# Performance work log

Hardware: AMD Instinct MI355X
Metric: run time of the kernel (lower is better)

## Reference

```python
import jax, jax.numpy as jnp
import numpy as np

B, S, D, H = 4, 2048, 2048, 16
HD = D // H          # 128, head_dim
THETA = 10000.0


def _rope_cos_sin(seq_len, head_dim, theta, dtype):
    # angle[t, j] = t * theta ** (-2j / head_dim), j = 0..head_dim//2-1
    inv_freq = theta ** (-jnp.arange(0, head_dim, 2, dtype=jnp.float32) / head_dim)
    ang = jnp.arange(seq_len, dtype=jnp.float32)[:, None] * inv_freq[None, :]  # [S, HD/2]
    # broadcast over heads: [S, 1, HD/2]
    return jnp.cos(ang)[:, None, :].astype(dtype), jnp.sin(ang)[:, None, :].astype(dtype)


def _apply_rope(t, cos, sin):
    # t: [B, S, H, HD]; complex mult on adjacent pairs (even=real, odd=imag)
    tr, ti = t[..., 0::2], t[..., 1::2]              # [B, S, H, HD/2]
    or_ = tr * cos - ti * sin
    oi_ = tr * sin + ti * cos
    return jnp.stack([or_, oi_], axis=-1).reshape(t.shape)


def setup_inputs() -> dict:
    key = jax.random.key(0)
    k1, k2, k3, k4, k5 = jax.random.split(key, 5)
    s = 1.0 / np.sqrt(D)
    return {
        "x": jax.random.normal(k1, (B, S, D), jnp.float32),
        "Wqkv": jax.random.normal(k2, (3 * D, D), jnp.float32) * s,
        "bqkv": jax.random.normal(k3, (3 * D,), jnp.float32) * 0.01,
        "Wo": jax.random.normal(k4, (D, D), jnp.float32) * s,
        "bo": jax.random.normal(k5, (D,), jnp.float32) * 0.01,
    }


def reference(x, Wqkv, bqkv, Wo, bo):
    b, s, d = x.shape
    qkv = x @ Wqkv.T + bqkv                          # [B, S, 3D]
    q, k, v = jnp.split(qkv, 3, axis=-1)
    q = q.reshape(b, s, H, HD)
    k = k.reshape(b, s, H, HD)
    v = v.reshape(b, s, H, HD)

    cos, sin = _rope_cos_sin(s, HD, THETA, x.dtype)
    q = _apply_rope(q, cos, sin)
    k = _apply_rope(k, cos, sin)

    # causal SDPA, scale = 1/sqrt(head_dim)
    scale = 1.0 / jnp.sqrt(jnp.asarray(HD, x.dtype))
    scores = jnp.einsum('bqhd,bkhd->bhqk', q, k) * scale
    causal = jnp.tril(jnp.ones((s, s), bool))
    scores = jnp.where(causal[None, None], scores, jnp.asarray(-jnp.inf, x.dtype))
    attn = jax.nn.softmax(scores, axis=-1)
    o = jnp.einsum('bhqk,bkhd->bqhd', attn, v).reshape(b, s, d)
    return o @ Wo.T + bo
```

## Files before the change

kernel.cpp:

```cpp
#include <hip/hip_runtime.h>
#include <hip/hip_bf16.h>
#include <math.h>

#define B_   4
#define S_   2048
#define D_   2048
#define H_   16
#define HD_  128
#define N3_  6144
#define M_   8192

typedef __attribute__((ext_vector_type(8))) short  short8;
typedef __attribute__((ext_vector_type(4))) float  float4_;

using bf16 = __hip_bfloat16;

static __device__ __forceinline__ float bf2f(bf16 v){ return __bfloat162float(v); }
static __device__ __forceinline__ bf16  f2bf(float v){ return __float2bfloat16(v); }
static __device__ __forceinline__ short f2bfs(float v){
    return (short)__builtin_bit_cast(unsigned short, __float2bfloat16(v));
}

static __device__ __forceinline__ short8 load8(const bf16* p){ return *(const short8*)p; }
static __device__ __forceinline__ short8 load8(const float* p){
    float4_ a = *(const float4_*)p;
    float4_ b = *(const float4_*)(p + 4);
    short8 r;
    r[0]=f2bfs(a[0]); r[1]=f2bfs(a[1]); r[2]=f2bfs(a[2]); r[3]=f2bfs(a[3]);
    r[4]=f2bfs(b[0]); r[5]=f2bfs(b[1]); r[6]=f2bfs(b[2]); r[7]=f2bfs(b[3]);
    return r;
}

static __device__ __forceinline__ void cp16_g2l(const void* g, void* l){
    __builtin_amdgcn_global_load_lds((const __attribute__((address_space(1))) void*)g,
                                     (__attribute__((address_space(3))) void*)l,
                                     16, 0, 0);
}

#define MFMA16 __builtin_amdgcn_mfma_f32_16x16x32_bf16

__global__ void cast_f32_bf16(const float* __restrict__ in, bf16* __restrict__ out, long n8){
    long i = (long)blockIdx.x * blockDim.x + threadIdx.x;
    if (i >= n8) return;
    *((short8*)out + i) = load8(in + 8*i);
}

template<typename AT, typename BT, typename OUT_T>
__global__ __launch_bounds__(256) void gemm_bt(const AT* __restrict__ A, int lda,
                                               const BT* __restrict__ Bt, int ldb,
                                               const float* __restrict__ bias,
                                               OUT_T* __restrict__ C, int ldc, int Kdim){
    __shared__ __align__(16) bf16 As[128*32];
    __shared__ __align__(16) bf16 Bs[128*32];
    const int tid  = threadIdx.x;
    const int lane = tid & 63;
    const int w    = tid >> 6;
    const int wm   = w >> 1, wn = w & 1;
    const int quad = lane >> 4, l15 = lane & 15;
    const int bn0  = blockIdx.x * 128, bm0 = blockIdx.y * 128;
    const int srow = tid >> 2;
    const int scol = (tid & 3) * 8;

    float4_ acc[4][4] = {};

    for (int k0 = 0; k0 < Kdim; k0 += 32){
        __syncthreads();
        #pragma unroll
        for (int half = 0; half < 2; ++half){
            int r = half*64 + srow;
            *(short8*)&As[r*32 + scol] = load8(&A[(size_t)(bm0 + r)*lda + k0 + scol]);
            *(short8*)&Bs[r*32 + scol] = load8(&Bt[(size_t)(bn0 + r)*ldb + k0 + scol]);
        }
        __syncthreads();
        short8 af[4], bfr[4];
        #pragma unroll
        for (int mt = 0; mt < 4; ++mt) af[mt]  = *(const short8*)&As[(wm*64 + mt*16 + l15)*32 + quad*8];
        #pragma unroll
        for (int nt = 0; nt < 4; ++nt) bfr[nt] = *(const short8*)&Bs[(wn*64 + nt*16 + l15)*32 + quad*8];
        #pragma unroll
        for (int mt = 0; mt < 4; ++mt)
            #pragma unroll
            for (int nt = 0; nt < 4; ++nt)
                acc[mt][nt] = MFMA16(af[mt], bfr[nt], acc[mt][nt], 0, 0, 0);
    }

    #pragma unroll
    for (int mt = 0; mt < 4; ++mt){
        int row = bm0 + wm*64 + mt*16 + quad*4;
        #pragma unroll
        for (int nt = 0; nt < 4; ++nt){
            int col = bn0 + wn*64 + nt*16 + l15;
            float bia = bias[col];
            #pragma unroll
            for (int r = 0; r < 4; ++r){
                float v = acc[mt][nt][r] + bia;
                size_t idx = (size_t)(row + r)*ldc + col;
                if constexpr (sizeof(OUT_T) == 2) ((bf16*)C)[idx] = f2bf(v);
                else                              ((float*)C)[idx] = v;
            }
        }
    }
}

template<typename OUT_T>
__global__ __launch_bounds__(512, 2) void gemm256(const bf16* __restrict__ A, int lda,
                                                  const bf16* __restrict__ Bt, int ldb,
                                                  const float* __restrict__ bias,
                                                  OUT_T* __restrict__ C, int ldc, int Kdim){
    __shared__ __align__(16) char lds[131072];
    const int tid  = threadIdx.x;
    const int lane = tid & 63;
    const int w    = tid >> 6;
    const int wm   = w >> 2, wn = w & 3;
    const int quad = lane >> 4, l15 = lane & 15;
    const int sw   = l15 & 7;
    const int bn0  = blockIdx.x * 256, bm0 = blockIdx.y * 256;

    const int g1 = tid, g2 = tid + 512;
    const int r1 = g1 >> 3, c1 = g1 & 7;
    const int r2 = g2 >> 3, c2 = g2 & 7;
    const int d1 = g1 * 16, d2 = g2 * 16;
    const char* pA0g1 = (const char*)(A  + (size_t)(bm0 +       r1)*lda + ((c1 ^ (r1 & 7)) << 3));
    const char* pA0g2 = (const char*)(A  + (size_t)(bm0 +       r2)*lda + ((c2 ^ (r2 & 7)) << 3));
    const char* pA1g1 = (const char*)(A  + (size_t)(bm0 + 128 + r1)*lda + ((c1 ^ (r1 & 7)) << 3));
    const char* pA1g2 = (const char*)(A  + (size_t)(bm0 + 128 + r2)*lda + ((c2 ^ (r2 & 7)) << 3));
    const char* pB0g1 = (const char*)(Bt + (size_t)(bn0 +       r1)*ldb + ((c1 ^ (r1 & 7)) << 3));
    const char* pB0g2 = (const char*)(Bt + (size_t)(bn0 +       r2)*ldb + ((c2 ^ (r2 & 7)) << 3));
    const char* pB1g1 = (const char*)(Bt + (size_t)(bn0 + 128 + r1)*ldb + ((c1 ^ (r1 & 7)) << 3));
    const char* pB1g2 = (const char*)(Bt + (size_t)(bn0 + 128 + r2)*ldb + ((c2 ^ (r2 & 7)) << 3));

    auto STAGE = [&](int bufb, int kby){
        cp16_g2l(pA0g1 + kby, lds + bufb +         d1);
        cp16_g2l(pA0g2 + kby, lds + bufb +         d2);
        cp16_g2l(pA1g1 + kby, lds + bufb + 16384 + d1);
        cp16_g2l(pA1g2 + kby, lds + bufb + 16384 + d2);
        cp16_g2l(pB0g1 + kby, lds + bufb + 32768 + d1);
        cp16_g2l(pB0g2 + kby, lds + bufb + 32768 + d2);
        cp16_g2l(pB1g1 + kby, lds + bufb + 49152 + d1);
        cp16_g2l(pB1g2 + kby, lds + bufb + 49152 + d2);
    };

    const int abase = (wm ? 16384 : 0);
    const int bbase = 32768 + ((wn >> 1) ? 16384 : 0);
    const int brow0 = (wn & 1) * 64;
    auto LDA = [&](int bufb, int mt, int kk) -> short8 {
        return *(const short8*)(lds + bufb + abase + (mt*16 + l15)*128
                                + (((kk*4 + quad) ^ sw) << 4));
    };
    auto LDB = [&](int bufb, int nt, int kk) -> short8 {
        return *(const short8*)(lds + bufb + bbase + (brow0 + nt*16 + l15)*128
                                + (((kk*4 + quad) ^ sw) << 4));
    };

    float4_ acc[8][4] = {};
    const int NT = Kdim >> 6;

    STAGE(0, 0);
    asm volatile("s_waitcnt vmcnt(0)" ::: "memory");
    __builtin_amdgcn_s_barrier();

    int cur = 0;
    for (int kt = 0; kt < NT; ++kt){
        const int bufb = cur << 16;
        if (kt + 1 < NT){
            STAGE(bufb ^ 65536, (kt + 1) << 7);
            asm volatile("s_waitcnt vmcnt(8)" ::: "memory");
        } else {
            asm volatile("s_waitcnt vmcnt(0)" ::: "memory");
        }
        __builtin_amdgcn_s_barrier();

        short8 af[4][2], bf[2][2], bg[2][2];
        #pragma unroll
        for (int mt = 0; mt < 4; ++mt){ af[mt][0] = LDA(bufb, mt, 0); af[mt][1] = LDA(bufb, mt, 1); }
        #pragma unroll
        for (int nt = 0; nt < 2; ++nt){ bf[nt][0] = LDB(bufb, nt, 0); bf[nt][1] = LDB(bufb, nt, 1); }
        __builtin_amdgcn_s_setprio(1);
        #pragma unroll
        for (int mt = 0; mt < 4; ++mt)
            #pragma unroll
            for (int nt = 0; nt < 2; ++nt){
                acc[mt][nt] = MFMA16(af[mt][0], bf[nt][0], acc[mt][nt], 0, 0, 0);
                acc[mt][nt] = MFMA16(af[mt][1], bf[nt][1], acc[mt][nt], 0, 0, 0);
            }
        __builtin_amdgcn_s_setprio(0);
        __builtin_amdgcn_s_barrier();
        #pragma unroll
        for (int nt = 0; nt < 2; ++nt){ bg[nt][0] = LDB(bufb, nt + 2, 0); bg[nt][1] = LDB(bufb, nt + 2, 1); }
        __builtin_amdgcn_s_setprio(1);
        #pragma unroll
        for (int mt = 0; mt < 4; ++mt)
            #pragma unroll
            for (int nt = 0; nt < 2; ++nt){
                acc[mt][nt+2] = MFMA16(af[mt][0], bg[nt][0], acc[mt][nt+2], 0, 0, 0);
                acc[mt][nt+2] = MFMA16(af[mt][1], bg[nt][1], acc[mt][nt+2], 0, 0, 0);
            }
        __builtin_amdgcn_s_setprio(0);
        __builtin_amdgcn_s_barrier();
        #pragma unroll
        for (int mt = 0; mt < 4; ++mt){ af[mt][0] = LDA(bufb, mt + 4, 0); af[mt][1] = LDA(bufb, mt + 4, 1); }
        __builtin_amdgcn_s_setprio(1);
        #pragma unroll
        for (int mt = 0; mt < 4; ++mt)
            #pragma unroll
            for (int nt = 0; nt < 2; ++nt){
                acc[mt+4][nt+2] = MFMA16(af[mt][0], bg[nt][0], acc[mt+4][nt+2], 0, 0, 0);
                acc[mt+4][nt+2] = MFMA16(af[mt][1], bg[nt][1], acc[mt+4][nt+2], 0, 0, 0);
            }
        __builtin_amdgcn_s_setprio(0);
        __builtin_amdgcn_s_barrier();
        __builtin_amdgcn_s_setprio(1);
        #pragma unroll
        for (int mt = 0; mt < 4; ++mt)
            #pragma unroll
            for (int nt = 0; nt < 2; ++nt){
                acc[mt+4][nt] = MFMA16(af[mt][0], bf[nt][0], acc[mt+4][nt], 0, 0, 0);
                acc[mt+4][nt] = MFMA16(af[mt][1], bf[nt][1], acc[mt+4][nt], 0, 0, 0);
            }
        __builtin_amdgcn_s_setprio(0);
        __builtin_amdgcn_s_barrier();
        cur ^= 1;
    }

    #pragma unroll
    for (int mt = 0; mt < 8; ++mt){
        int row = bm0 + wm*128 + mt*16 + quad*4;
        #pragma unroll
        for (int nt = 0; nt < 4; ++nt){
            int col = bn0 + wn*64 + nt*16 + l15;
            float bia = bias[col];
            #pragma unroll
            for (int r = 0; r < 4; ++r){
                float v = acc[mt][nt][r] + bia;
                size_t idx = (size_t)(row + r)*ldc + col;
                if constexpr (sizeof(OUT_T) == 2) ((bf16*)C)[idx] = f2bf(v);
                else                              ((float*)C)[idx] = v;
            }
        }
    }
}

__global__ void rope_apply(bf16* __restrict__ qkv){
    int idx = blockIdx.x * blockDim.x + threadIdx.x;
    int p = idx & 63;
    int h = (idx >> 6) & (H_-1);
    int s = (idx >> 10) & (S_-1);
    int b = idx >> 21;
    float freq = powf(10000.0f, -(float)(2*p) / (float)HD_);
    float ang = (float)s * freq;
    float c = cosf(ang), sn = sinf(ang);
    size_t base = (size_t)(b*S_ + s) * N3_ + h*HD_ + 2*p;
    float tr = bf2f(qkv[base]), ti = bf2f(qkv[base+1]);
    qkv[base]   = f2bf(tr*c - ti*sn);
    qkv[base+1] = f2bf(tr*sn + ti*c);
    size_t kb = base + D_;
    tr = bf2f(qkv[kb]); ti = bf2f(qkv[kb+1]);
    qkv[kb]   = f2bf(tr*c - ti*sn);
    qkv[kb+1] = f2bf(tr*sn + ti*c);
}

struct KV { short8 k0, k1, v0, v1; };

__global__ __launch_bounds__(512, 2) void attn(bf16* __restrict__ QKV){
    const int bid  = blockIdx.x;
    const int xcd  = bid & 7, slot = bid >> 3;
    const int bh   = xcd*8 + (slot & 7);
    const int tp   = slot >> 3;
    const int b = bh >> 4, h = bh & 15;
    const int tid = threadIdx.x;
    const int w = tid >> 6, lane = tid & 63, quad = lane >> 4, l15 = lane & 15;
    bf16* Qp = QKV + (size_t)b*S_*N3_ + h*HD_;
    const bf16* Kp = Qp + D_;
    const bf16* Vp = Qp + 2*D_;
    __shared__ __align__(16) bf16 Ks[64*128];
    __shared__ __align__(16) bf16 Vt[128*64];
    __shared__ __align__(16) bf16 Pls[8*16*64];

    const int skey = tid >> 3;
    const int st   = tid & 7;
    const int kswz = (skey & 7) << 4;

    const float scale2 = 0.12751707470412558f;

    auto load_kv = [&](int kb) -> KV {
        KV r;
        const char* krow = (const char*)&Kp[(size_t)(kb + skey)*N3_];
        const char* vrow = (const char*)&Vp[(size_t)(kb + skey)*N3_];
        r.k0 = *(const short8*)(krow + st*32);
        r.k1 = *(const short8*)(krow + st*32 + 16);
        r.v0 = *(const short8*)(vrow + st*32);
        r.v1 = *(const short8*)(vrow + st*32 + 16);
        return r;
    };
    auto stage_write = [&](KV x){
        *(short8*)((char*)Ks + ((skey*256 + st*32     ) ^ kswz)) = x.k0;
        *(short8*)((char*)Ks + ((skey*256 + st*32 + 16) ^ kswz)) = x.k1;
        #pragma unroll
        for (int g = 0; g < 2; ++g){
            short8 vv = g ? x.v1 : x.v0;
            #pragma unroll
            for (int j = 0; j < 8; ++j){
                const int d = st*16 + g*8 + j;
                *(short*)((char*)Vt + ((d*128 + skey*2)
                          ^ (((j ^ (st >> 1)) & 7) << 4))) = vv[j];
            }
        }
    };

    KV a = load_kv(0);
    KV bset;

    for (int half = 0; half < 2; ++half){
        const int t = half ? (15 - tp) : tp;
        const int qrow = t*128 + w*16 + l15;
        short8 qf[4];
        #pragma unroll
        for (int kc = 0; kc < 4; ++kc)
            qf[kc] = *(const short8*)&Qp[(size_t)qrow*N3_ + kc*32 + quad*8];

        float4_ accO[8] = {};
        float m_i[4], l_i[4];
        #pragma unroll
        for (int r = 0; r < 4; ++r){ m_i[r] = -3.0e38f; l_i[r] = 0.0f; }
        const int rbase = t*128 + w*16 + quad*4;
        const int wmax  = t*128 + w*16 + 15;
        const int nch = 2*t + 2;
        const int nch1 = 32 - 2*tp;
        auto kb_of = [&](int s){ return (half ? (nch - 1 - s) : s) * 64; };

        auto compute = [&](int kb){
            float4_ sacc[4] = {};
            __builtin_amdgcn_s_setprio(1);
            #pragma unroll
            for (int kc = 0; kc < 4; ++kc)
                #pragma unroll
                for (int nt = 0; nt < 4; ++nt){
                    short8 kf = *(const short8*)((const char*)Ks +
                        (((nt*16 + l15)*256 + kc*64 + quad*16) ^ ((l15 & 7) << 4)));
                    sacc[nt] = MFMA16(qf[kc], kf, sacc[nt], 0, 0, 0);
                }
            __builtin_amdgcn_s_setprio(0);

            #pragma unroll
            for (int nt = 0; nt < 4; ++nt){
                const int j = kb + nt*16 + l15;
                #pragma unroll
                for (int r = 0; r < 4; ++r){
                    float v = sacc[nt][r] * scale2;
                    sacc[nt][r] = (j > rbase + r) ? -3.0e38f : v;
                }
            }

            float alpha[4];
            #pragma unroll
            for (int r = 0; r < 4; ++r){
                float v = fmaxf(fmaxf(sacc[0][r], sacc[1][r]), fmaxf(sacc[2][r], sacc[3][r]));
                v = fmaxf(v, m_i[r]);
                #pragma unroll
                for (int off = 1; off < 16; off <<= 1) v = fmaxf(v, __shfl_xor(v, off, 64));
                alpha[r] = exp2f(m_i[r] - v);
                m_i[r] = v;
                float s = 0.0f;
                #pragma unroll
                for (int nt = 0; nt < 4; ++nt){
                    float p = exp2f(sacc[nt][r] - v);
                    sacc[nt][r] = p; s += p;
                }
                #pragma unroll
                for (int off = 1; off < 16; off <<= 1) s += __shfl_xor(s, off, 64);
                l_i[r] = l_i[r]*alpha[r] + s;
            }
            #pragma unroll
            for (int dt = 0; dt < 8; ++dt)
                #pragma unroll
                for (int r = 0; r < 4; ++r) accO[dt][r] *= alpha[r];

            #pragma unroll
            for (int nt = 0; nt < 4; ++nt)
                #pragma unroll
                for (int r = 0; r < 4; ++r){
                    const int prow = quad*4 + r;
                    *(short*)((char*)Pls + ((w*2048 + prow*128 + (nt*16 + l15)*2)
                                            ^ ((prow & 7) << 4))) = f2bfs(sacc[nt][r]);
                }
            __asm volatile("s_waitcnt lgkmcnt(0)" ::: "memory");
            short8 pf0 = *(const short8*)((const char*)Pls +
                ((w*2048 + l15*128      + quad*16) ^ ((l15 & 7) << 4)));
            short8 pf1 = *(const short8*)((const char*)Pls +
                ((w*2048 + l15*128 + 64 + quad*16) ^ ((l15 & 7) << 4)));

            __builtin_amdgcn_s_setprio(1);
            #pragma unroll
            for (int dt = 0; dt < 8; ++dt){
                const int rb = (dt*16 + l15)*128;
                const int sw2 = (((l15 & 7) ^ (dt >> 1)) & 7) << 4;
                short8 vf0 = *(const short8*)((const char*)Vt + ((rb      + quad*16) ^ sw2));
                short8 vf1 = *(const short8*)((const char*)Vt + ((rb + 64 + quad*16) ^ sw2));
                accO[dt] = MFMA16(pf0, vf0, accO[dt], 0, 0, 0);
                accO[dt] = MFMA16(pf1, vf1, accO[dt], 0, 0, 0);
            }
            __builtin_amdgcn_s_setprio(0);
        };

        for (int s = 0; s < nch; s += 2){
            __syncthreads();
            stage_write(a);
            bset = load_kv(kb_of(s + 1));
            __syncthreads();
            { const int kb0 = kb_of(s); if (kb0 <= wmax) compute(kb0); }

            __syncthreads();
            stage_write(bset);
            if (s + 2 < nch)      a = load_kv(kb_of(s + 2));
            else if (half == 0)   a = load_kv((nch1 - 1) * 64);
            __syncthreads();
            { const int kb1 = kb_of(s + 1); if (kb1 <= wmax) compute(kb1); }
        }

        float inv[4];
        #pragma unroll
        for (int r = 0; r < 4; ++r) inv[r] = 1.0f / l_i[r];
        #pragma unroll
        for (int dt = 0; dt < 8; ++dt)
            #pragma unroll
            for (int r = 0; r < 4; ++r){
                int s = t*128 + w*16 + quad*4 + r;
                int d = dt*16 + l15;
                Qp[(size_t)s*N3_ + d] = f2bf(accO[dt][r]*inv[r]);
            }
    }
}

extern "C" void kernel_launch(void* const* d_in, const int* in_sizes, int n_in,
                              void* d_out, int out_size, void* d_ws, size_t ws_size,
                              hipStream_t stream){
    const float* x    = (const float*)d_in[0];
    const float* Wqkv = (const float*)d_in[1];
    const float* bqkv = (const float*)d_in[2];
    const float* Wo   = (const float*)d_in[3];
    const float* bo   = (const float*)d_in[4];
    float* out = (float*)d_out;
    char* ws = (char*)d_ws;

    bf16* qkv = (bf16*)(ws + 0);

    const size_t OFF_XB = 100663296, OFF_WQ = 134217728, OFF_WO = 159383552;
    const bool big = (ws_size >= (size_t)167772160);

    if (big){
        bf16* xb    = (bf16*)(ws + OFF_XB);
        bf16* wqkvb = (bf16*)(ws + OFF_WQ);
        bf16* wob   = (bf16*)(ws + OFF_WO);
        long n8;
        n8 = (long)M_*D_/8;   cast_f32_bf16<<<(n8+255)/256, 256, 0, stream>>>(x, xb, n8);
        n8 = (long)N3_*D_/8;  cast_f32_bf16<<<(n8+255)/256, 256, 0, stream>>>(Wqkv, wqkvb, n8);
        n8 = (long)D_*D_/8;   cast_f32_bf16<<<(n8+255)/256, 256, 0, stream>>>(Wo, wob, n8);
        gemm256<bf16><<<dim3(N3_/256, M_/256), 512, 0, stream>>>(
            xb, D_, wqkvb, D_, bqkv, qkv, N3_, D_);
        rope_apply<<<(B_*S_*H_*64)/256, 256, 0, stream>>>(qkv);
        attn<<<dim3(512), 512, 0, stream>>>(qkv);
        gemm256<float><<<dim3(D_/256, M_/256), 512, 0, stream>>>(
            qkv, N3_, wob, D_, bo, out, D_, D_);
    } else {
        gemm_bt<float,float,bf16><<<dim3(N3_/128, M_/128), 256, 0, stream>>>(
            x, D_, Wqkv, D_, bqkv, qkv, N3_, D_);
        rope_apply<<<(B_*S_*H_*64)/256, 256, 0, stream>>>(qkv);
        attn<<<dim3(512), 512, 0, stream>>>(qkv);
        gemm_bt<bf16,float,float><<<dim3(D_/128, M_/128), 256, 0, stream>>>(
            qkv, N3_, Wo, D_, bo, out, D_, D_);
    }
}
```

Baseline: 651.9 us.

## Double-buffer K/V in LDS, lazy softmax rescale, skip mask on full tiles

Adds a second LDS buffer for K and V so each key chunk needs one barrier instead of two, overlapping staging with compute. Softmax now skips the max reduction, rescale and accumulator multiply when the new tile max stays within a threshold of the running max. Row sums are reduced across lanes once at the end. The causal mask is applied only on diagonal tiles, and the swizzles for P and V are changed. The cost is doubled K/V LDS use, which may limit occupancy, plus added branch divergence checks.

```diff
diff --git a/kernel.cpp b/kernel.cpp
--- a/kernel.cpp
+++ b/kernel.cpp
@@ -272,8 +272,8 @@
     bf16* Qp = QKV + (size_t)b*S_*N3_ + h*HD_;
     const bf16* Kp = Qp + D_;
     const bf16* Vp = Qp + 2*D_;
-    __shared__ __align__(16) bf16 Ks[64*128];
-    __shared__ __align__(16) bf16 Vt[128*64];
+    __shared__ __align__(16) bf16 Ks[2*64*128];
+    __shared__ __align__(16) bf16 Vt[2*128*64];
     __shared__ __align__(16) bf16 Pls[8*16*64];
 
     const int skey = tid >> 3;
@@ -292,23 +292,24 @@
         r.v1 = *(const short8*)(vrow + st*32 + 16);
         return r;
     };
-    auto stage_write = [&](KV x){
-        *(short8*)((char*)Ks + ((skey*256 + st*32     ) ^ kswz)) = x.k0;
-        *(short8*)((char*)Ks + ((skey*256 + st*32 + 16) ^ kswz)) = x.k1;
+    auto stage_write = [&](int pbuf, KV x){
+        char* kd = (char*)Ks + pbuf*16384;
+        char* vd = (char*)Vt + pbuf*16384;
+        *(short8*)(kd + ((skey*256 + st*32     ) ^ kswz)) = x.k0;
+        *(short8*)(kd + ((skey*256 + st*32 + 16) ^ kswz)) = x.k1;
         #pragma unroll
         for (int g = 0; g < 2; ++g){
             short8 vv = g ? x.v1 : x.v0;
             #pragma unroll
             for (int j = 0; j < 8; ++j){
                 const int d = st*16 + g*8 + j;
-                *(short*)((char*)Vt + ((d*128 + skey*2)
-                          ^ (((j ^ (st >> 1)) & 7) << 4))) = vv[j];
+                *(short*)(vd + ((d*128 + skey*2) ^ (((j ^ st) & 7) << 4))) = vv[j];
             }
         }
     };
 
+    int pb = 0;
     KV a = load_kv(0);
-    KV bset;
 
     for (int half = 0; half < 2; ++half){
         const int t = half ? (15 - tp) : tp;
@@ -323,103 +324,132 @@
         #pragma unroll
         for (int r = 0; r < 4; ++r){ m_i[r] = -3.0e38f; l_i[r] = 0.0f; }
         const int rbase = t*128 + w*16 + quad*4;
-        const int wmax  = t*128 + w*16 + 15;
+        const int wmin  = t*128 + w*16;
+        const int wmax  = wmin + 15;
         const int nch = 2*t + 2;
         const int nch1 = 32 - 2*tp;
         auto kb_of = [&](int s){ return (half ? (nch - 1 - s) : s) * 64; };
 
-        auto compute = [&](int kb){
+        auto compute = [&](int pbuf, int kb){
+            const char* kbs = (const char*)Ks + pbuf*16384;
+            const char* vbs = (const char*)Vt + pbuf*16384;
             float4_ sacc[4] = {};
             __builtin_amdgcn_s_setprio(1);
             #pragma unroll
             for (int kc = 0; kc < 4; ++kc)
                 #pragma unroll
                 for (int nt = 0; nt < 4; ++nt){
-                    short8 kf = *(const short8*)((const char*)Ks +
+                    short8 kf = *(const short8*)(kbs +
                         (((nt*16 + l15)*256 + kc*64 + quad*16) ^ ((l15 & 7) << 4)));
                     sacc[nt] = MFMA16(qf[kc], kf, sacc[nt], 0, 0, 0);
                 }
             __builtin_amdgcn_s_setprio(0);
 
-            #pragma unroll
-            for (int nt = 0; nt < 4; ++nt){
-                const int j = kb + nt*16 + l15;
+            if (kb + 63 > wmin){
+                #pragma unroll
+                for (int nt = 0; nt < 4; ++nt){
+                    const int j = kb + nt*16 + l15;
+                    #pragma unroll
+                    for (int r = 0; r < 4; ++r){
+                        float v = sacc[nt][r] * scale2;
+                        sacc[nt][r] = (j > rbase + r) ? -3.0e38f : v;
+                    }
+                }
+            } else {
+                #pragma unroll
+                for (int nt = 0; nt < 4; ++nt)
+                    #pragma unroll
+                    for (int r = 0; r < 4; ++r) sacc[nt][r] *= scale2;
+            }
+
+            float tmax[4];
+            #pragma unroll
+            for (int r = 0; r < 4; ++r)
+                tmax[r] = fmaxf(fmaxf(sacc[0][r], sacc[1][r]),
+                                fmaxf(sacc[2][r], sacc[3][r]));
+            int stable = (tmax[0] <= m_i[0] + 8.0f) & (tmax[1] <= m_i[1] + 8.0f) &
+                         (tmax[2] <= m_i[2] + 8.0f) & (tmax[3] <= m_i[3] + 8.0f);
+            if (__all(stable)){
                 #pragma unroll
                 for (int r = 0; r < 4; ++r){
-                    float v = sacc[nt][r] * scale2;
-                    sacc[nt][r] = (j > rbase + r) ? -3.0e38f : v;
+                    float s = 0.0f;
+                    #pragma unroll
+                    for (int nt = 0; nt < 4; ++nt){
+                        float p = exp2f(sacc[nt][r] - m_i[r]);
+                        sacc[nt][r] = p; s += p;
+                    }
+                    l_i[r] += s;
                 }
-            }
-
-            float alpha[4];
-            #pragma unroll
-            for (int r = 0; r < 4; ++r){
-                float v = fmaxf(fmaxf(sacc[0][r], sacc[1][r]), fmaxf(sacc[2][r], sacc[3][r]));
-                v = fmaxf(v, m_i[r]);
-                #pragma unroll
-                for (int off = 1; off < 16; off <<= 1) v = fmaxf(v, __shfl_xor(v, off, 64));
-                alpha[r] = exp2f(m_i[r] - v);
-                m_i[r] = v;
-                float s = 0.0f;
-                #pragma unroll
-                for (int nt = 0; nt < 4; ++nt){
-                    float p = exp2f(sacc[nt][r] - v);
-                    sacc[nt][r] = p; s += p;
+            } else {
+                float alpha[4];
+                #pragma unroll
+                for (int r = 0; r < 4; ++r){
+                    float v = fmaxf(tmax[r], m_i[r]);
+                    #pragma unroll
+                    for (int off = 1; off < 16; off <<= 1) v = fmaxf(v, __shfl_xor(v, off, 64));
+                    alpha[r] = exp2f(m_i[r] - v);
+                    m_i[r] = v;
+                    float s = 0.0f;
+                    #pragma unroll
+                    for (int nt = 0; nt < 4; ++nt){
+                        float p = exp2f(sacc[nt][r] - v);
+                        sacc[nt][r] = p; s += p;
+                    }
+                    l_i[r] = l_i[r]*alpha[r] + s;
                 }
                 #pragma unroll
-                for (int off = 1; off < 16; off <<= 1) s += __shfl_xor(s, off, 64);
-                l_i[r] = l_i[r]*alpha[r] + s;
-            }
-            #pragma unroll
-            for (int dt = 0; dt < 8; ++dt)
-                #pragma unroll
-                for (int r = 0; r < 4; ++r) accO[dt][r] *= alpha[r];
+                for (int dt = 0; dt < 8; ++dt)
+                    #pragma unroll
+                    for (int r = 0; r < 4; ++r) accO[dt][r] *= alpha[r];
+            }
 
             #pragma unroll
             for (int nt = 0; nt < 4; ++nt)
                 #pragma unroll
                 for (int r = 0; r < 4; ++r){
                     const int prow = quad*4 + r;
+                    const int swp = ((prow & 7) ^ (((prow >> 3) & 1) << 1)) << 4;
                     *(short*)((char*)Pls + ((w*2048 + prow*128 + (nt*16 + l15)*2)
-                                            ^ ((prow & 7) << 4))) = f2bfs(sacc[nt][r]);
+                                            ^ swp)) = f2bfs(sacc[nt][r]);
                 }
             __asm volatile("s_waitcnt lgkmcnt(0)" ::: "memory");
+            const int swr = ((l15 & 7) ^ (((l15 >> 3) & 1) << 1)) << 4;
             short8 pf0 = *(const short8*)((const char*)Pls +
-                ((w*2048 + l15*128      + quad*16) ^ ((l15 & 7) << 4)));
+                ((w*2048 + l15*128      + quad*16) ^ swr));
             short8 pf1 = *(const short8*)((const char*)Pls +
-                ((w*2048 + l15*128 + 64 + quad*16) ^ ((l15 & 7) << 4)));
+                ((w*2048 + l15*128 + 64 + quad*16) ^ swr));
 
             __builtin_amdgcn_s_setprio(1);
             #pragma unroll
             for (int dt = 0; dt < 8; ++dt){
                 const int rb = (dt*16 + l15)*128;
-                const int sw2 = (((l15 & 7) ^ (dt >> 1)) & 7) << 4;
-                short8 vf0 = *(const short8*)((const char*)Vt + ((rb      + quad*16) ^ sw2));
-                short8 vf1 = *(const short8*)((const char*)Vt + ((rb + 64 + quad*16) ^ sw2));
+                const int sw2 = (((l15 & 7) ^ dt) & 7) << 4;
+                short8 vf0 = *(const short8*)(vbs + ((rb      + quad*16) ^ sw2));
+                short8 vf1 = *(const short8*)(vbs + ((rb + 64 + quad*16) ^ sw2));
                 accO[dt] = MFMA16(pf0, vf0, accO[dt], 0, 0, 0);
                 accO[dt] = MFMA16(pf1, vf1, accO[dt], 0, 0, 0);
             }
             __builtin_amdgcn_s_setprio(0);
         };
 
-        for (int s = 0; s < nch; s += 2){
-            __syncthreads();
-            stage_write(a);
-            bset = load_kv(kb_of(s + 1));
-            __syncthreads();
-            { const int kb0 = kb_of(s); if (kb0 <= wmax) compute(kb0); }
-
-            __syncthreads();
-            stage_write(bset);
-            if (s + 2 < nch)      a = load_kv(kb_of(s + 2));
+        for (int s = 0; s < nch; ++s){
+            stage_write(pb, a);
+            if (s + 1 < nch)      a = load_kv(kb_of(s + 1));
             else if (half == 0)   a = load_kv((nch1 - 1) * 64);
-            __syncthreads();
-            { const int kb1 = kb_of(s + 1); if (kb1 <= wmax) compute(kb1); }
+            asm volatile("s_waitcnt lgkmcnt(0)" ::: "memory");
+            __builtin_amdgcn_s_barrier();
+            { const int kb = kb_of(s); if (kb <= wmax) compute(pb, kb); }
+            pb ^= 1;
         }
 
         float inv[4];
         #pragma unroll
-        for (int r = 0; r < 4; ++r) inv[r] = 1.0f / l_i[r];
+        for (int r = 0; r < 4; ++r){
+            float s = l_i[r];
+            #pragma unroll
+            for (int off = 1; off < 16; off <<= 1) s += __shfl_xor(s, off, 64);
+            inv[r] = 1.0f / s;
+        }
         #pragma unroll
         for (int dt = 0; dt < 8; ++dt)
             #pragma unroll
```

After: 604.5 us. -7.3%, faster.
